# Kernel optimization log

Hardware: AMD Instinct MI355X
Metric: run time of the kernel (lower is better)

The kernel has to match this reference:

```python
import jax, jax.numpy as jnp
import numpy as np

N = 400_000      # total nodes
E = 6_400_000    # intra edges (avg degree 16)
B = 128          # graphs in batch
D = 35           # node_dim (pinned by the code)
DH = 2 * D       # 70 = attention dim
T = 140          # padded sequence length
SEQ = 2          # cat(lig,pro) [B,70] -> view(B,-1,35) => seq_len 2

# mask construction from forward() with sequence.size(1) == 2 (constant)
_m = np.eye(T, dtype=bool)
_m[SEQ:, :] = False
_m[:, SEQ:] = False
_m[:, SEQ - 1] = True
_m[SEQ - 1, :] = True
_m[SEQ - 1, SEQ - 1] = False
MASK = jnp.asarray(_m)  # [T,T] bool, broadcast over batch


def setup_inputs() -> dict:
    k = jax.random.split(jax.random.key(0), 24)
    s = 0.1
    return {
        "x": jax.random.normal(k[0], (N, D), jnp.float32),
        "edge_index": jax.random.randint(k[1], (2, E), 0, N),
        "split": jax.random.randint(k[2], (N,), 0, 2),
        "batch": jnp.sort(jax.random.randint(k[3], (N,), 0, B)),
        # 5 protein + 5 ligand GCNConv layers (weight [in,out], bias)
        "Wp": jax.random.normal(k[4], (5, D, D), jnp.float32) * s,
        "bp": jnp.zeros((5, D), jnp.float32),
        "Wl": jax.random.normal(k[5], (5, D, D), jnp.float32) * s,
        "bl": jnp.zeros((5, D), jnp.float32),
        # BiLSTM (torch layout: [4H, in]/[4H, H], gate order i,f,g,o)
        "wif": jax.random.normal(k[6], (4 * D, D), jnp.float32) * s,
        "whf": jax.random.normal(k[7], (4 * D, D), jnp.float32) * s,
        "bif": jnp.zeros((4 * D,), jnp.float32),
        "bhf": jnp.zeros((4 * D,), jnp.float32),
        "wib": jax.random.normal(k[8], (4 * D, D), jnp.float32) * s,
        "whb": jax.random.normal(k[9], (4 * D, D), jnp.float32) * s,
        "bib": jnp.zeros((4 * D,), jnp.float32),
        "bhb": jnp.zeros((4 * D,), jnp.float32),
        # single-head self-attention (70 -> 70) q/k/v/out projections
        "Wq": jax.random.normal(k[10], (DH, DH), jnp.float32) * s,
        "bq": jnp.zeros((DH,), jnp.float32),
        "Wk": jax.random.normal(k[11], (DH, DH), jnp.float32) * s,
        "bk": jnp.zeros((DH,), jnp.float32),
        "Wv": jax.random.normal(k[12], (DH, DH), jnp.float32) * s,
        "bv": jnp.zeros((DH,), jnp.float32),
        "Wo": jax.random.normal(k[13], (DH, DH), jnp.float32) * s,
        "bo": jnp.zeros((DH,), jnp.float32),
        # fc_in: Linear(9800,4340) + BatchNorm1d(4340) + Mish; fc_out: Linear(4340,1)
        "W1": jax.random.normal(k[14], (4340, 9800), jnp.float32) * 0.01,
        "b1": jnp.zeros((4340,), jnp.float32),
        "gamma": jnp.ones((4340,), jnp.float32),
        "beta": jnp.zeros((4340,), jnp.float32),
        "W2": jax.random.normal(k[15], (1, 4340), jnp.float32) * s,
        "b2": jnp.zeros((1,), jnp.float32),
    }


def _gcn_stack(x, src, dst, ew, Ws, bs):
    """5 stacked GCNConv + ReLU over a masked edge set (ew in {0,1} per edge).
    Matches PyG GCNConv: sym-normalized A+I, deg counted on active edges."""
    deg = jax.ops.segment_sum(ew, dst, num_segments=N) + 1.0  # +1 self loop
    dinv = jax.lax.rsqrt(deg)
    ecoef = (ew * dinv[src] * dinv[dst])[:, None]  # [E,1]
    scoef = (dinv * dinv)[:, None]                 # self-loop norm [N,1]
    h = x
    for i in range(5):
        t = h @ Ws[i]  # [N,D]
        agg = jax.ops.segment_sum(t[src] * ecoef, dst, num_segments=N)
        h = jax.nn.relu(agg + t * scoef + bs[i])
    return h


def _lstm(seq, wih, whh, b, reverse):
    # seq: [T, Bt, D] -> hidden states [T, Bt, D]
    def step(carry, xt):
        h, c = carry
        g = xt @ wih.T + h @ whh.T + b
        i, f, gg, o = jnp.split(g, 4, axis=-1)
        c = jax.nn.sigmoid(f) * c + jax.nn.sigmoid(i) * jnp.tanh(gg)
        h = jax.nn.sigmoid(o) * jnp.tanh(c)
        return (h, c), h
    h0 = jnp.zeros((seq.shape[1], D), seq.dtype)
    _, hs = jax.lax.scan(step, (h0, h0), seq, reverse=reverse)
    return hs


def _mish(x):
    return x * jnp.tanh(jax.nn.softplus(x))


def reference(x, edge_index, split, batch, Wp, bp, Wl, bl,
              wif, whf, bif, bhf, wib, whb, bib, bhb,
              Wq, bq, Wk, bk, Wv, bv, Wo, bo,
              W1, b1, gamma, beta, W2, b2):
    src, dst = edge_index[0], edge_index[1]
    wpro = (split[src] == 1).astype(x.dtype)  # edges whose source is protein
    wlig = 1.0 - wpro                          # edges whose source is ligand

    feat_pro = _gcn_stack(x, src, dst, wpro, Wp, bp)
    feat_lig = _gcn_stack(x, src, dst, wlig, Wl, bl)

    pro = jax.ops.segment_sum(feat_pro, batch, num_segments=B)  # [B,35]
    lig = jax.ops.segment_sum(feat_lig, batch, num_segments=B)

    seq = jnp.concatenate([lig, pro], axis=1).reshape(B, SEQ, D)  # [B,2,35]
    seq = jnp.pad(seq, ((0, 0), (0, T - SEQ), (0, 0)))            # [B,140,35]
    seq = seq.transpose(1, 0, 2)                                   # [T,B,35]

    hf = _lstm(seq, wif, whf, bif + bhf, False)
    hb = _lstm(seq, wib, whb, bib + bhb, True)
    out = jnp.concatenate([hf, hb], axis=-1).transpose(1, 0, 2)   # [B,140,70]

    q = out @ Wq.T + bq
    k = out @ Wk.T + bk
    v = out @ Wv.T + bv
    scores = jnp.einsum('btd,bsd->bts', q, k) / jnp.sqrt(jnp.float32(DH))
    scores = jnp.where(MASK, scores, jnp.float32(-1e9))
    ctx = jax.nn.softmax(scores, axis=-1) @ v                     # [B,140,70]
    ctx = ctx @ Wo.T + bo

    y = ctx.reshape(B, -1) @ W1.T + b1                            # [B,4340]
    mu = y.mean(0)
    var = ((y - mu) ** 2).mean(0)
    y = (y - mu) * jax.lax.rsqrt(var + 1e-5) * gamma + beta       # BN train mode
    y = _mish(y)
    return (y @ W2.T + b2).reshape(-1)                             # [B]
```

## Files before the change

kernel.cpp:

```cpp
#include <hip/hip_runtime.h>
#include <hip/hip_fp16.h>
#include <math.h>

#define DD 35
#define TT 140
#define DHX 70
#define GW 36
#define SLOT 48

__device__ __forceinline__ float sigf(float x){ return 1.0f/(1.0f+expf(-x)); }

__global__ void k_init(unsigned int* packed, int* bstart, int* bend,
                       float* out, const float* b2, int N, int B){
  int i = blockIdx.x*blockDim.x + threadIdx.x;
  if (i < N){ packed[i]=0u; }
  if (i < B){ bstart[i] = 0x7fffffff; bend[i] = 0; out[i] = b2[0]; }
}

__global__ void k_bitf(const int* __restrict__ split, unsigned int* bitf, int NW, int N){
  int w = blockIdx.x*blockDim.x + threadIdx.x;
  if (w >= NW) return;
  unsigned int m = 0;
  int base = w*32;
  int lim = N - base; if (lim > 32) lim = 32;
  for (int j=0;j<lim;++j) m |= (split[base+j]==1 ? 1u : 0u) << j;
  bitf[w] = m;
}

__global__ void k_fill2(const int* __restrict__ ei, const unsigned int* __restrict__ bitf,
                        unsigned int* packed, int* eidx, int E){
  int e = blockIdx.x*blockDim.x + threadIdx.x;
  if (e >= E) return;
  int s = __builtin_nontemporal_load(ei+e);
  int d = __builtin_nontemporal_load(ei+E+e);
  unsigned int bit = (bitf[s>>5] >> (s&31)) & 1u;
  unsigned int old = atomicAdd(&packed[d], bit ? 0x10000u : 1u);
  int slot = (int)((old>>16) + (old&0xFFFFu));
  if (slot < SLOT) eidx[(size_t)d*SLOT + slot] = (s<<1) | (int)bit;
}

__global__ void k_node1(const unsigned int* __restrict__ packed,
                        float* dinvp, float* dinvl,
                        const int* __restrict__ batch,
                        int* bstart, int* bend, int N){
  int i = blockIdx.x*blockDim.x + threadIdx.x;
  if (i >= N) return;
  unsigned int p = packed[i];
  int pc = (int)(p >> 16), lc = (int)(p & 0xFFFFu);
  dinvp[i] = rsqrtf((float)(pc + 1));
  dinvl[i] = rsqrtf((float)(lc + 1));
  int b = batch[i];
  if (i == 0 || batch[i-1] != b) bstart[b] = i;
  if (i == N-1 || batch[i+1] != b) bend[b] = i + 1;
}

__global__ void __launch_bounds__(256)
k_pack0(const float* __restrict__ x, const float* __restrict__ dinvp,
        const float* __restrict__ dinvl, const int* __restrict__ split,
        __half* __restrict__ gg, __half* __restrict__ own, int N){
  int node = blockIdx.x*4 + (threadIdx.x>>6);
  if (node >= N) return;
  int ln = threadIdx.x & 63;
  float v = (ln < DD)? x[(size_t)node*DD + ln] : 0.f;
  float dp = dinvp[node], dl = dinvl[node];
  int sel = split[node];
  float gv = (sel? dp : dl)*v;
  float ov = (sel? dl : dp)*v;
  float g0 = __shfl(gv,(2*ln)&63,64), g1 = __shfl(gv,(2*ln+1)&63,64);
  float o0 = __shfl(ov,(2*ln)&63,64), o1 = __shfl(ov,(2*ln+1)&63,64);
  if (ln < 18){
    *(__half2*)(gg  + (size_t)node*GW + 2*ln) = __floats2half2_rn(g0,g1);
    *(__half2*)(own + (size_t)node*GW + 2*ln) = __floats2half2_rn(o0,o1);
  }
}

__global__ void __launch_bounds__(256)
k_gcn(const __half* __restrict__ gg, const __half* __restrict__ own,
      __half* __restrict__ ggo, __half* __restrict__ owno,
      __half* __restrict__ hpF, __half* __restrict__ hlF,
      const unsigned int* __restrict__ packed, const int* __restrict__ eidx,
      const int* __restrict__ split,
      const float* __restrict__ dinvp, const float* __restrict__ dinvl,
      const float* __restrict__ Wp, const float* __restrict__ bp,
      const float* __restrict__ Wl, const float* __restrict__ bl,
      int N, int last){
  int node = blockIdx.x*4 + (threadIdx.x>>6);
  if (node >= N) return;
  int ln = threadIdx.x & 63;
  int sub = ln & 15, eo = ln >> 4;
  unsigned int pk = packed[node];
  int total = (int)((pk>>16) + (pk&0xFFFFu));
  if (total > SLOT) total = SLOT;
  int e0 = node*SLOT, e1 = e0 + total;
  float2 ap = {0.f,0.f}, al = {0.f,0.f};
  float2 tp = {0.f,0.f}, tl = {0.f,0.f};
  for (int e = e0; e < e1; e += 4){
    int idx = e + eo;
    bool val = idx < e1;
    int enc = val ? eidx[idx] : 0;
    const char* row = (const char*)gg + (size_t)(enc>>1)*(GW*2);
    unsigned int u = 0, ut = 0;
    if (val) u = *(const unsigned int*)(row + 4*sub);
    if (val && sub < 2) ut = *(const unsigned int*)(row + 64 + 4*sub);
    float ms = (val && (enc & 1)) ? 1.f : 0.f;
    float mo = (val && !(enc & 1)) ? 1.f : 0.f;
    float2 f  = __half22float2(*(__half2*)&u);
    float2 ft = __half22float2(*(__half2*)&ut);
    ap.x += ms*f.x;  ap.y += ms*f.y;  al.x += mo*f.x;  al.y += mo*f.y;
    tp.x += ms*ft.x; tp.y += ms*ft.y; tl.x += mo*ft.x; tl.y += mo*ft.y;
  }
  for (int off=16; off<64; off<<=1){
    ap.x += __shfl_xor(ap.x,off,64); ap.y += __shfl_xor(ap.y,off,64);
    al.x += __shfl_xor(al.x,off,64); al.y += __shfl_xor(al.y,off,64);
    tp.x += __shfl_xor(tp.x,off,64); tp.y += __shfl_xor(tp.y,off,64);
    tl.x += __shfl_xor(tl.x,off,64); tl.y += __shfl_xor(tl.y,off,64);
  }
  int srcl = ln>>1, odd = ln&1;
  float px = __shfl(ap.x, srcl, 64), py = __shfl(ap.y, srcl, 64);
  float lx = __shfl(al.x, srcl, 64), ly = __shfl(al.y, srcl, 64);
  float zp = odd? py : px;
  float zl = odd? ly : lx;
  float tpx0 = __shfl(tp.x,0,64), tpy0 = __shfl(tp.y,0,64), tpx1 = __shfl(tp.x,1,64);
  float tlx0 = __shfl(tl.x,0,64), tly0 = __shfl(tl.y,0,64), tlx1 = __shfl(tl.x,1,64);
  if (ln == 32){ zp = tpx0; zl = tlx0; }
  else if (ln == 33){ zp = tpy0; zl = tly0; }
  else if (ln == 34){ zp = tpx1; zl = tlx1; }
  int sel = split[node];
  float dp = dinvp[node], dl = dinvl[node];
  float sg = 0.f, so = 0.f;
  if (ln < DD){
    sg = __half2float(gg [(size_t)node*GW + ln]);
    so = __half2float(own[(size_t)node*GW + ln]);
  }
  float selfp = sel ? sg : so;
  float selfl = sel ? so : sg;
  bool act = ln < DD;
  float zpf = act ? dp*(zp + selfp) : 0.f;
  float zlf = act ? dl*(zl + selfl) : 0.f;
  float op = 0.f, ol = 0.f;
  for (int j=0;j<DD;++j){
    float zpj = __shfl(zpf, j, 64);
    float zlj = __shfl(zlf, j, 64);
    float wp = act ? Wp[j*DD+ln] : 0.f;
    float wl = act ? Wl[j*DD+ln] : 0.f;
    op += zpj*wp; ol += zlj*wl;
  }
  float opb = act ? fmaxf(op + bp[ln], 0.f) : 0.f;
  float olb = act ? fmaxf(ol + bl[ln], 0.f) : 0.f;
  if (last){
    float a0 = __shfl(opb,(2*ln)&63,64), a1 = __shfl(opb,(2*ln+1)&63,64);
    float b0 = __shfl(olb,(2*ln)&63,64), b1 = __shfl(olb,(2*ln+1)&63,64);
    if (ln < 18){
      *(__half2*)(hpF + (size_t)node*GW + 2*ln) = __floats2half2_rn(a0,a1);
      *(__half2*)(hlF + (size_t)node*GW + 2*ln) = __floats2half2_rn(b0,b1);
    }
  } else {
    float ggv  = sel ? dp*opb : dl*olb;
    float ownv = sel ? dl*olb : dp*opb;
    float a0 = __shfl(ggv,(2*ln)&63,64), a1 = __shfl(ggv,(2*ln+1)&63,64);
    float b0 = __shfl(ownv,(2*ln)&63,64), b1 = __shfl(ownv,(2*ln+1)&63,64);
    if (ln < 18){
      *(__half2*)(ggo  + (size_t)node*GW + 2*ln) = __floats2half2_rn(a0,a1);
      *(__half2*)(owno + (size_t)node*GW + 2*ln) = __floats2half2_rn(b0,b1);
    }
  }
}

__global__ void k_bsum(const __half* __restrict__ gp, const __half* __restrict__ gl,
                       const int* __restrict__ bstart, const int* __restrict__ bend,
                       float* pro, float* lig){
  __shared__ float sp[4][GW], sl[4][GW];
  int b = blockIdx.x;
  int w = threadIdx.x>>6, ln = threadIdx.x&63;
  int s0 = bstart[b], s1 = bend[b];
  float apx=0.f, apy=0.f, alx=0.f, aly=0.f;
  if (ln < 18){
    for (int n=s0+w; n<s1; n+=4){
      float2 a = __half22float2(*(const __half2*)(gp + (size_t)n*GW + 2*ln));
      float2 c = __half22float2(*(const __half2*)(gl + (size_t)n*GW + 2*ln));
      apx+=a.x; apy+=a.y; alx+=c.x; aly+=c.y;
    }
    sp[w][2*ln]=apx; sp[w][2*ln+1]=apy;
    sl[w][2*ln]=alx; sl[w][2*ln+1]=aly;
  }
  __syncthreads();
  if (threadIdx.x < DD){
    int d = threadIdx.x;
    pro[b*DD+d] = sp[0][d]+sp[1][d]+sp[2][d]+sp[3][d];
    lig[b*DD+d] = sl[0][d]+sl[1][d]+sl[2][d]+sl[3][d];
  }
}

__global__ void k_lstm_common(const float* __restrict__ wib, const float* __restrict__ whb,
                              const float* __restrict__ bib, const float* __restrict__ bhb,
                              float* hbc, float* hbcst){
  __shared__ float h[DD], cc[DD], g[4*DD];
  int t = threadIdx.x;
  if (t < DD){ h[t]=0.f; cc[t]=0.f; }
  __syncthreads();
  for (int k=1;k<=TT-2;++k){
    if (t < 4*DD){
      float acc = bib[t]+bhb[t];
      for (int m=0;m<DD;++m) acc += whb[t*DD+m]*h[m];
      g[t]=acc;
    }
    __syncthreads();
    if (t < DD){
      float ig=g[t], fg=g[DD+t], gg=g[2*DD+t], og=g[3*DD+t];
      float cv = sigf(fg)*cc[t] + sigf(ig)*tanhf(gg);
      float hv = sigf(og)*tanhf(cv);
      cc[t]=cv; h[t]=hv;
      hbc[(TT-k)*DD + t] = hv;
    }
    __syncthreads();
  }
  if (t<DD){ hbcst[t]=h[t]; hbcst[DD+t]=cc[t]; }
}

__global__ void k_lstm_batch(const float* __restrict__ lig, const float* __restrict__ pro,
   const float* __restrict__ wif, const float* __restrict__ whf,
   const float* __restrict__ bif, const float* __restrict__ bhf,
   const float* __restrict__ wib, const float* __restrict__ whb,
   const float* __restrict__ bib, const float* __restrict__ bhb,
   const float* __restrict__ hbc, const float* __restrict__ hbcst, float* outseq){
  __shared__ float x0[DD], x1[DD], h[DD], cc[DD], g[4*DD], xg0[4*DD], xg1[4*DD];
  int b = blockIdx.x, t = threadIdx.x;
  if (t<DD){ x0[t]=lig[b*DD+t]; x1[t]=pro[b*DD+t]; h[t]=0.f; cc[t]=0.f; }
  __syncthreads();
  if (t<4*DD){
    float a0=0.f, a1=0.f;
    for (int m=0;m<DD;++m){ a0 += wif[t*DD+m]*x0[m]; a1 += wif[t*DD+m]*x1[m]; }
    xg0[t]=a0; xg1[t]=a1;
  }
  __syncthreads();
  float* outb = outseq + (size_t)b*TT*DHX;
  for (int tt=0;tt<TT;++tt){
    if (t<4*DD){
      float acc = bif[t]+bhf[t] + (tt==0? xg0[t] : (tt==1? xg1[t] : 0.f));
      for (int m=0;m<DD;++m) acc += whf[t*DD+m]*h[m];
      g[t]=acc;
    }
    __syncthreads();
    if (t<DD){
      float ig=g[t], fg=g[DD+t], gg=g[2*DD+t], og=g[3*DD+t];
      float cv = sigf(fg)*cc[t]+sigf(ig)*tanhf(gg);
      float hv = sigf(og)*tanhf(cv);
      cc[t]=cv; h[t]=hv;
      outb[tt*DHX + t] = hv;
    }
    __syncthreads();
  }
  if (t<4*DD){
    float a0=0.f, a1=0.f;
    for (int m=0;m<DD;++m){ a0 += wib[t*DD+m]*x0[m]; a1 += wib[t*DD+m]*x1[m]; }
    xg0[t]=a0; xg1[t]=a1;
  }
  if (t<DD){ h[t]=hbcst[t]; cc[t]=hbcst[DD+t]; }
  __syncthreads();
  for (int step=0; step<2; ++step){
    int tt = 1-step;
    if (t<4*DD){
      float acc = bib[t]+bhb[t] + (tt==1? xg1[t] : xg0[t]);
      for (int m=0;m<DD;++m) acc += whb[t*DD+m]*h[m];
      g[t]=acc;
    }
    __syncthreads();
    if (t<DD){
      float ig=g[t], fg=g[DD+t], gg=g[2*DD+t], og=g[3*DD+t];
      float cv = sigf(fg)*cc[t]+sigf(ig)*tanhf(gg);
      float hv = sigf(og)*tanhf(cv);
      cc[t]=cv; h[t]=hv;
      outb[tt*DHX + DD + t] = hv;
    }
    __syncthreads();
  }
  for (int idx=t; idx<(TT-2)*DD; idx+=blockDim.x){
    int tt = 2 + idx/DD, d = idx%DD;
    outb[tt*DHX + DD + d] = hbc[tt*DD + d];
  }
}

__global__ void __launch_bounds__(256)
k_attn(const float* __restrict__ outseq,
  const float* __restrict__ Wq, const float* __restrict__ bq,
  const float* __restrict__ Wk, const float* __restrict__ bk,
  const float* __restrict__ Wv, const float* __restrict__ bv,
  const float* __restrict__ Wo, const float* __restrict__ bo,
  float* PT, int B){
  __shared__ float so[TT*DHX];
  __shared__ float sk[TT*DHX];
  __shared__ float sv[TT*DHX];
  __shared__ float sq[2*DHX];
  __shared__ float es[TT];
  __shared__ float red[4];
  __shared__ float ctx[3*DHX];
  int b = blockIdx.x, tid = threadIdx.x;
  const float* ob = outseq + (size_t)b*TT*DHX;
  for (int i=tid;i<TT*DHX;i+=256) so[i]=ob[i];
  __syncthreads();
  for (int i=tid;i<TT*DHX;i+=256){
    int s=i/DHX, d=i%DHX;
    float ak=bk[d], av=bv[d];
    const float* r = so + s*DHX;
    for (int j=0;j<DHX;++j){ float o=r[j]; ak += o*Wk[d*DHX+j]; av += o*Wv[d*DHX+j]; }
    sk[i]=ak; sv[i]=av;
  }
  for (int i=tid;i<2*DHX;i+=256){
    int s=i/DHX, d=i%DHX;
    float a=bq[d];
    for (int j=0;j<DHX;++j) a += so[s*DHX+j]*Wq[d*DHX+j];
    sq[i]=a;
  }
  __syncthreads();
  const float scale = 0.11952286093343936f;
  for (int s=tid;s<TT;s+=256){
    float a=0.f;
    for (int j=0;j<DHX;++j) a += sq[DHX+j]*sk[s*DHX+j];
    es[s] = a*scale;
  }
  __syncthreads();
  if (tid < 64){
    float m=-1e30f;
    for (int s=tid;s<TT;s+=64) if (s!=1) m=fmaxf(m, es[s]);
    for (int o=32;o;o>>=1) m = fmaxf(m, __shfl_xor(m,o,64));
    if (tid==0) red[0]=m;
  }
  __syncthreads();
  float m = red[0];
  for (int s=tid;s<TT;s+=256) es[s] = (s==1)? 0.f : expf(es[s]-m);
  __syncthreads();
  if (tid<64){
    float sum=0.f;
    for (int s=tid;s<TT;s+=64) sum+=es[s];
    for (int o=32;o;o>>=1) sum += __shfl_xor(sum,o,64);
    if (tid==0) red[1]=sum;
  }
  if (tid==0){
    float s00=0.f,s01=0.f;
    for (int j=0;j<DHX;++j){ s00 += sq[j]*sk[j]; s01 += sq[j]*sk[DHX+j]; }
    s00*=scale; s01*=scale;
    float mm=fmaxf(s00,s01);
    float e0=expf(s00-mm), e1=expf(s01-mm);
    red[2]=e0/(e0+e1); red[3]=e1/(e0+e1);
  }
  __syncthreads();
  float inv = 1.0f/red[1];
  float a0=red[2], a1=red[3];
  if (tid < DHX){
    int d=tid;
    float c1=0.f;
    for (int s=0;s<TT;++s) c1 += es[s]*sv[s*DHX+d];
    ctx[DHX+d] = c1*inv;
    ctx[d] = a0*sv[d] + a1*sv[DHX+d];
    ctx[2*DHX+d] = sv[DHX+d];
  }
  __syncthreads();
  for (int i=tid;i<3*DHX;i+=256){
    int tt=i/DHX, d=i%DHX;
    float a=bo[d];
    const float* cv = ctx + tt*DHX;
    for (int j=0;j<DHX;++j) a += Wo[d*DHX+j]*cv[j];
    PT[(size_t)i*B + b] = a;
  }
}

__global__ void k_w1s(const float* __restrict__ W1, float* w1s){
  __shared__ float sh[DHX];
  int j = blockIdx.x; int tid = threadIdx.x;
  int d = tid % DHX, half = tid / DHX;
  const float* r = W1 + (size_t)j*(TT*DHX);
  float acc = 0.f;
  int t0 = half ? 71 : 2, t1 = half ? 140 : 71;
  for (int t=t0; t<t1; ++t) acc += r[t*DHX+d];
  if (half==0) sh[d] = acc;
  __syncthreads();
  if (half) w1s[(size_t)j*DHX+d] = sh[d] + acc;
}

__global__ void k_y(const float* __restrict__ PT, const float* __restrict__ W1,
                    const float* __restrict__ w1s, const float* __restrict__ b1,
                    float* yT, int B){
  int j = blockIdx.x; int b = threadIdx.x;
  const float* r = W1 + (size_t)j*(TT*DHX);
  float acc = b1[j];
  for (int i=0;i<2*DHX;++i) acc += r[i]*PT[(size_t)i*B+b];
  const float* rs = w1s + (size_t)j*DHX;
  for (int i=0;i<DHX;++i) acc += rs[i]*PT[(size_t)(2*DHX+i)*B+b];
  yT[(size_t)j*B+b] = acc;
}

__global__ void k_bn(const float* __restrict__ yT, const float* __restrict__ gamma,
                     const float* __restrict__ beta, const float* __restrict__ W2,
                     float* out, int B, int J){
  __shared__ float red_s[2];
  int b = threadIdx.x;
  int lane = b & 63, w = b>>6;
  float acc = 0.f;
  int j0 = blockIdx.x*32;
  float invB = 1.0f/(float)B;
  for (int jj=0;jj<32;++jj){
    int j = j0+jj; if (j>=J) break;
    float v = yT[(size_t)j*B + b];
    float s=v;
    for (int o=32;o;o>>=1) s += __shfl_xor(s,o,64);
    if (lane==0) red_s[w]=s;
    __syncthreads();
    float mu = (red_s[0]+red_s[1]) * invB;
    __syncthreads();
    float dd = v-mu;
    float q=dd*dd;
    for (int o=32;o;o>>=1) q += __shfl_xor(q,o,64);
    if (lane==0) red_s[w]=q;
    __syncthreads();
    float var = (red_s[0]+red_s[1]) * invB;
    __syncthreads();
    float xn = dd*rsqrtf(var+1e-5f)*gamma[j]+beta[j];
    float sp = (xn>20.f)? xn : log1pf(expf(xn));
    float mish = xn*tanhf(sp);
    acc += mish*W2[j];
  }
  atomicAdd(&out[b], acc);
}

extern "C" void kernel_launch(void* const* d_in, const int* in_sizes, int n_in,
                              void* d_out, int out_size, void* d_ws, size_t ws_size,
                              hipStream_t stream)
{
  const float* x    = (const float*)d_in[0];
  const int*   ei   = (const int*)  d_in[1];
  const int*   split= (const int*)  d_in[2];
  const int*   batch= (const int*)  d_in[3];
  const float* Wp   = (const float*)d_in[4];
  const float* bp   = (const float*)d_in[5];
  const float* Wl   = (const float*)d_in[6];
  const float* bl   = (const float*)d_in[7];
  const float* wif  = (const float*)d_in[8];
  const float* whf  = (const float*)d_in[9];
  const float* bif  = (const float*)d_in[10];
  const float* bhf  = (const float*)d_in[11];
  const float* wib  = (const float*)d_in[12];
  const float* whb  = (const float*)d_in[13];
  const float* bib  = (const float*)d_in[14];
  const float* bhb  = (const float*)d_in[15];
  const float* Wq   = (const float*)d_in[16];
  const float* bq   = (const float*)d_in[17];
  const float* Wk   = (const float*)d_in[18];
  const float* bk   = (const float*)d_in[19];
  const float* Wv   = (const float*)d_in[20];
  const float* bv   = (const float*)d_in[21];
  const float* Wo   = (const float*)d_in[22];
  const float* bo   = (const float*)d_in[23];
  const float* W1   = (const float*)d_in[24];
  const float* b1   = (const float*)d_in[25];
  const float* gam  = (const float*)d_in[26];
  const float* bet  = (const float*)d_in[27];
  const float* W2   = (const float*)d_in[28];
  const float* b2   = (const float*)d_in[29];
  float* out = (float*)d_out;

  const int N = in_sizes[0]/DD;
  const int E = in_sizes[1]/2;
  const int B = out_size;
  const int J = in_sizes[25];
  (void)n_in; (void)ws_size;

  char* ws = (char*)d_ws;
  size_t off_ = 0;
  auto carve = [&](size_t bytes)->void*{ void* p = ws + off_; off_ = (off_ + bytes + 255) & ~(size_t)255; return p; };
  __half* ggA  = (__half*)carve((size_t)N*GW*2);
  __half* ownA = (__half*)carve((size_t)N*GW*2);
  __half* ggB  = (__half*)carve((size_t)N*GW*2);
  __half* ownB = (__half*)carve((size_t)N*GW*2);
  int*   eidx  = (int*)  carve((size_t)N*SLOT*4);
  float* dinvp = (float*)carve((size_t)N*4);
  float* dinvl = (float*)carve((size_t)N*4);
  unsigned int* packed = (unsigned int*)carve((size_t)N*4);
  unsigned int* bitf   = (unsigned int*)carve((size_t)((N+31)/32)*4);
  float* pro   = (float*)carve((size_t)B*DD*4);
  float* lig   = (float*)carve((size_t)B*DD*4);
  int*   bstart= (int*)  carve((size_t)B*4);
  int*   bend  = (int*)  carve((size_t)B*4);
  float* hbc   = (float*)carve((size_t)TT*DD*4);
  float* hbcst = (float*)carve(2*DD*4);
  float* outseq= (float*)carve((size_t)B*TT*DHX*4);
  float* PT    = (float*)carve((size_t)3*DHX*B*4);
  float* w1s   = (float*)carve((size_t)J*DHX*4);
  float* yT    = (float*)carve((size_t)J*B*4);

  int mx = (N>B)?N:B;
  int NW = (N+31)/32;
  k_init<<<(mx+255)/256, 256, 0, stream>>>(packed, bstart, bend, out, b2, N, B);
  k_bitf<<<(NW+255)/256, 256, 0, stream>>>(split, bitf, NW, N);
  k_fill2<<<(E+255)/256, 256, 0, stream>>>(ei, bitf, packed, eidx, E);
  k_node1<<<(N+255)/256, 256, 0, stream>>>(packed, dinvp, dinvl, batch, bstart, bend, N);
  k_pack0<<<(N+3)/4, 256, 0, stream>>>(x, dinvp, dinvl, split, ggA, ownA, N);

  const __half* ggi = ggA; const __half* owni = ownA;
  __half* ggo = ggB; __half* owno = ownB;
  __half* hpF = nullptr; __half* hlF = nullptr;
  for (int L=0; L<5; ++L){
    int last = (L==4);
    if (last){ hpF = ggo; hlF = owno; }
    k_gcn<<<(N+3)/4, 256, 0, stream>>>(ggi, owni, ggo, owno, ggo, owno,
      packed, eidx, split, dinvp, dinvl,
      Wp + (size_t)L*DD*DD, bp + (size_t)L*DD, Wl + (size_t)L*DD*DD, bl + (size_t)L*DD,
      N, last);
    const __half* t1 = ggi; ggi = ggo; ggo = (__half*)t1;
    const __half* t2 = owni; owni = owno; owno = (__half*)t2;
  }

  k_bsum<<<B, 256, 0, stream>>>(hpF, hlF, bstart, bend, pro, lig);
  k_lstm_common<<<1, 192, 0, stream>>>(wib, whb, bib, bhb, hbc, hbcst);
  k_lstm_batch<<<B, 192, 0, stream>>>(lig, pro, wif, whf, bif, bhf, wib, whb, bib, bhb, hbc, hbcst, outseq);
  k_attn<<<B, 256, 0, stream>>>(outseq, Wq, bq, Wk, bk, Wv, bv, Wo, bo, PT, B);
  k_w1s<<<J, 140, 0, stream>>>(W1, w1s);
  k_y<<<J, B, 0, stream>>>(PT, W1, w1s, b1, yT, B);
  k_bn<<<(J+31)/32, B, 0, stream>>>(yT, gam, bet, W2, out, B, J);
}
```

Baseline: 3.817 ms.

## Pack gathered GCN features into 64-byte block-floating-point rows

Replaces the fp16 gathered-feature rows (72 bytes) with a custom per-row shared-exponent format: 14-bit integer mantissas packed two per 32-bit word, plus a 4-bit exponent and nibble-packed tail columns, for 64 bytes per row. The edge-gather loop does one aligned 4-byte load per lane and decodes with integer shifts, aiming to cut gather bandwidth and load count. The final-layer outputs go to separate buffers. The cost is extra encode and decode arithmetic, and reduced precision, especially for the three tail features.

```diff
diff --git a/kernel.cpp b/kernel.cpp
--- a/kernel.cpp
+++ b/kernel.cpp
@@ -9,6 +9,26 @@
 #define SLOT 48
 
 __device__ __forceinline__ float sigf(float x){ return 1.0f/(1.0f+expf(-x)); }
+
+__device__ __forceinline__ void encode_row(float v, int ln, unsigned int* dst){
+  float av = fabsf(v);
+  for (int o=32;o;o>>=1) av = fmaxf(av, __shfl_xor(av,o,64));
+  int e = ((__float_as_int(av)>>23)&255) - 127;
+  int Ep = e < -8 ? -8 : (e > 7 ? 7 : e);
+  float invs = __int_as_float((139 - Ep)<<23);
+  int m = (int)rintf(v*invs);
+  m = m < -8191 ? -8191 : (m > 8191 ? 8191 : m);
+  int mt = (int)rintf(v*invs*0.25f) + 2048;
+  mt = mt < 0 ? 0 : (mt > 4095 ? 4095 : mt);
+  int mB  = __shfl(m, (ln+16)&63, 64);
+  int t32 = __shfl(mt, 32, 64), t33 = __shfl(mt, 33, 64), t34 = __shfl(mt, 34, 64);
+  if (ln < 16){
+    int tt = (ln<3)? t32 : (ln<6)? t33 : t34;
+    int p  = (ln<3)? ln : (ln<6)? ln-3 : ln-6;
+    int nib = (ln<9) ? ((tt>>(4*p))&15) : (ln==15 ? (Ep+8) : 0);
+    dst[ln] = ((unsigned)m & 0x3FFFu) | (((unsigned)mB & 0x3FFFu)<<14) | ((unsigned)nib<<28);
+  }
+}
 
 __global__ void k_init(unsigned int* packed, int* bstart, int* bend,
                        float* out, const float* b2, int N, int B){
@@ -57,7 +77,7 @@
 __global__ void __launch_bounds__(256)
 k_pack0(const float* __restrict__ x, const float* __restrict__ dinvp,
         const float* __restrict__ dinvl, const int* __restrict__ split,
-        __half* __restrict__ gg, __half* __restrict__ own, int N){
+        unsigned int* __restrict__ gg, __half* __restrict__ own, int N){
   int node = blockIdx.x*4 + (threadIdx.x>>6);
   if (node >= N) return;
   int ln = threadIdx.x & 63;
@@ -66,17 +86,14 @@
   int sel = split[node];
   float gv = (sel? dp : dl)*v;
   float ov = (sel? dl : dp)*v;
-  float g0 = __shfl(gv,(2*ln)&63,64), g1 = __shfl(gv,(2*ln+1)&63,64);
+  encode_row((ln<DD)? gv : 0.f, ln, gg + (size_t)node*16);
   float o0 = __shfl(ov,(2*ln)&63,64), o1 = __shfl(ov,(2*ln+1)&63,64);
-  if (ln < 18){
-    *(__half2*)(gg  + (size_t)node*GW + 2*ln) = __floats2half2_rn(g0,g1);
-    *(__half2*)(own + (size_t)node*GW + 2*ln) = __floats2half2_rn(o0,o1);
-  }
+  if (ln < 18) *(__half2*)(own + (size_t)node*GW + 2*ln) = __floats2half2_rn(o0,o1);
 }
 
 __global__ void __launch_bounds__(256)
-k_gcn(const __half* __restrict__ gg, const __half* __restrict__ own,
-      __half* __restrict__ ggo, __half* __restrict__ owno,
+k_gcn(const unsigned int* __restrict__ gg, const __half* __restrict__ own,
+      unsigned int* __restrict__ ggo, __half* __restrict__ owno,
       __half* __restrict__ hpF, __half* __restrict__ hlF,
       const unsigned int* __restrict__ packed, const int* __restrict__ eidx,
       const int* __restrict__ split,
@@ -87,51 +104,63 @@
   int node = blockIdx.x*4 + (threadIdx.x>>6);
   if (node >= N) return;
   int ln = threadIdx.x & 63;
-  int sub = ln & 15, eo = ln >> 4;
+  int sub = ln & 15;
+  int grp = ln >> 4;
   unsigned int pk = packed[node];
   int total = (int)((pk>>16) + (pk&0xFFFFu));
   if (total > SLOT) total = SLOT;
   int e0 = node*SLOT, e1 = e0 + total;
-  float2 ap = {0.f,0.f}, al = {0.f,0.f};
-  float2 tp = {0.f,0.f}, tl = {0.f,0.f};
+
+  float aP0=0.f, aP1=0.f, aL0=0.f, aL1=0.f;
+  float aPt=0.f, aLt=0.f;
   for (int e = e0; e < e1; e += 4){
-    int idx = e + eo;
+    int idx = e + grp;
     bool val = idx < e1;
     int enc = val ? eidx[idx] : 0;
-    const char* row = (const char*)gg + (size_t)(enc>>1)*(GW*2);
-    unsigned int u = 0, ut = 0;
-    if (val) u = *(const unsigned int*)(row + 4*sub);
-    if (val && sub < 2) ut = *(const unsigned int*)(row + 64 + 4*sub);
-    float ms = (val && (enc & 1)) ? 1.f : 0.f;
-    float mo = (val && !(enc & 1)) ? 1.f : 0.f;
-    float2 f  = __half22float2(*(__half2*)&u);
-    float2 ft = __half22float2(*(__half2*)&ut);
-    ap.x += ms*f.x;  ap.y += ms*f.y;  al.x += mo*f.x;  al.y += mo*f.y;
-    tp.x += ms*ft.x; tp.y += ms*ft.y; tl.x += mo*ft.x; tl.y += mo*ft.y;
+    unsigned int u = val ? gg[(size_t)(enc>>1)*16 + sub] : 0u;
+    int uE = __shfl((int)u, (ln & 48) | 15, 64);
+    float s = val ? __int_as_float(((((unsigned)uE)>>28) + 107) << 23) : 0.f;
+    float sp = (enc & 1) ? s : 0.f;
+    float sl = (enc & 1) ? 0.f : s;
+    int m0 = ((int)(u<<18))>>18;
+    int m1 = ((int)(u<<4))>>18;
+    float f0 = (float)m0, f1 = (float)m1;
+    aP0 += sp*f0; aP1 += sp*f1; aL0 += sl*f0; aL1 += sl*f1;
+    float nv = (sub == 9) ? 1.0f : (float)(u>>28);
+    aPt += sp*nv; aLt += sl*nv;
   }
   for (int off=16; off<64; off<<=1){
-    ap.x += __shfl_xor(ap.x,off,64); ap.y += __shfl_xor(ap.y,off,64);
-    al.x += __shfl_xor(al.x,off,64); al.y += __shfl_xor(al.y,off,64);
-    tp.x += __shfl_xor(tp.x,off,64); tp.y += __shfl_xor(tp.y,off,64);
-    tl.x += __shfl_xor(tl.x,off,64); tl.y += __shfl_xor(tl.y,off,64);
-  }
-  int srcl = ln>>1, odd = ln&1;
-  float px = __shfl(ap.x, srcl, 64), py = __shfl(ap.y, srcl, 64);
-  float lx = __shfl(al.x, srcl, 64), ly = __shfl(al.y, srcl, 64);
-  float zp = odd? py : px;
-  float zl = odd? ly : lx;
-  float tpx0 = __shfl(tp.x,0,64), tpy0 = __shfl(tp.y,0,64), tpx1 = __shfl(tp.x,1,64);
-  float tlx0 = __shfl(tl.x,0,64), tly0 = __shfl(tl.y,0,64), tlx1 = __shfl(tl.x,1,64);
-  if (ln == 32){ zp = tpx0; zl = tlx0; }
-  else if (ln == 33){ zp = tpy0; zl = tly0; }
-  else if (ln == 34){ zp = tpx1; zl = tlx1; }
+    aP0 += __shfl_xor(aP0,off,64); aP1 += __shfl_xor(aP1,off,64);
+    aL0 += __shfl_xor(aL0,off,64); aL1 += __shfl_xor(aL1,off,64);
+    aPt += __shfl_xor(aPt,off,64); aLt += __shfl_xor(aLt,off,64);
+  }
+  float a0 = __shfl(aP0, ln&15, 64), a1 = __shfl(aP1, ln&15, 64);
+  float b0 = __shfl(aL0, ln&15, 64), b1 = __shfl(aL1, ln&15, 64);
+  int tb = (ln>=32 && ln<35) ? (ln-32)*3 : 0;
+  float q0p=__shfl(aPt,tb,64), q1p=__shfl(aPt,tb+1,64), q2p=__shfl(aPt,tb+2,64);
+  float q0l=__shfl(aLt,tb,64), q1l=__shfl(aLt,tb+1,64), q2l=__shfl(aLt,tb+2,64);
+  float Sp = __shfl(aPt, 9, 64), Sl = __shfl(aLt, 9, 64);
+  float vtp = 4.f*(q0p + 16.f*q1p + 256.f*q2p - 2048.f*Sp);
+  float vtl = 4.f*(q0l + 16.f*q1l + 256.f*q2l - 2048.f*Sl);
+  float zp = (ln<16)? a0 : (ln<32)? a1 : vtp;
+  float zl = (ln<16)? b0 : (ln<32)? b1 : vtl;
   int sel = split[node];
   float dp = dinvp[node], dl = dinvl[node];
+  const unsigned int* rowS = gg + (size_t)node*16;
+  unsigned int wE = rowS[15];
+  float ss = __int_as_float((int)(((wE>>28) + 107) << 23));
   float sg = 0.f, so = 0.f;
-  if (ln < DD){
-    sg = __half2float(gg [(size_t)node*GW + ln]);
-    so = __half2float(own[(size_t)node*GW + ln]);
-  }
+  if (ln < 32){
+    unsigned int w = rowS[sub];
+    int m = (ln<16)? (((int)(w<<18))>>18) : (((int)(w<<4))>>18);
+    sg = (float)m * ss;
+  } else if (ln < DD){
+    int t = ln-32;
+    unsigned int w0=rowS[3*t], w1=rowS[3*t+1], w2=rowS[3*t+2];
+    int mp = (int)(w0>>28) | ((int)(w1>>28)<<4) | ((int)(w2>>28)<<8);
+    sg = (float)(mp - 2048) * ss * 4.f;
+  }
+  if (ln < DD) so = __half2float(own[(size_t)node*GW + ln]);
   float selfp = sel ? sg : so;
   float selfl = sel ? so : sg;
   bool act = ln < DD;
@@ -148,21 +177,19 @@
   float opb = act ? fmaxf(op + bp[ln], 0.f) : 0.f;
   float olb = act ? fmaxf(ol + bl[ln], 0.f) : 0.f;
   if (last){
-    float a0 = __shfl(opb,(2*ln)&63,64), a1 = __shfl(opb,(2*ln+1)&63,64);
-    float b0 = __shfl(olb,(2*ln)&63,64), b1 = __shfl(olb,(2*ln+1)&63,64);
+    float c0 = __shfl(opb,(2*ln)&63,64), c1 = __shfl(opb,(2*ln+1)&63,64);
+    float d0 = __shfl(olb,(2*ln)&63,64), d1 = __shfl(olb,(2*ln+1)&63,64);
     if (ln < 18){
-      *(__half2*)(hpF + (size_t)node*GW + 2*ln) = __floats2half2_rn(a0,a1);
-      *(__half2*)(hlF + (size_t)node*GW + 2*ln) = __floats2half2_rn(b0,b1);
+      *(__half2*)(hpF + (size_t)node*GW + 2*ln) = __floats2half2_rn(c0,c1);
+      *(__half2*)(hlF + (size_t)node*GW + 2*ln) = __floats2half2_rn(d0,d1);
     }
   } else {
     float ggv  = sel ? dp*opb : dl*olb;
     float ownv = sel ? dl*olb : dp*opb;
-    float a0 = __shfl(ggv,(2*ln)&63,64), a1 = __shfl(ggv,(2*ln+1)&63,64);
-    float b0 = __shfl(ownv,(2*ln)&63,64), b1 = __shfl(ownv,(2*ln+1)&63,64);
-    if (ln < 18){
-      *(__half2*)(ggo  + (size_t)node*GW + 2*ln) = __floats2half2_rn(a0,a1);
-      *(__half2*)(owno + (size_t)node*GW + 2*ln) = __floats2half2_rn(b0,b1);
-    }
+    encode_row(act? ggv : 0.f, ln, ggo + (size_t)node*16);
+    float d0 = __shfl(ownv,(2*ln)&63,64), d1 = __shfl(ownv,(2*ln+1)&63,64);
+    if (ln < 18)
+      *(__half2*)(owno + (size_t)node*GW + 2*ln) = __floats2half2_rn(d0,d1);
   }
 }
 
@@ -467,10 +494,12 @@
   char* ws = (char*)d_ws;
   size_t off_ = 0;
   auto carve = [&](size_t bytes)->void*{ void* p = ws + off_; off_ = (off_ + bytes + 255) & ~(size_t)255; return p; };
-  __half* ggA  = (__half*)carve((size_t)N*GW*2);
+  unsigned int* ggA = (unsigned int*)carve((size_t)N*16*4);
+  unsigned int* ggB = (unsigned int*)carve((size_t)N*16*4);
   __half* ownA = (__half*)carve((size_t)N*GW*2);
-  __half* ggB  = (__half*)carve((size_t)N*GW*2);
   __half* ownB = (__half*)carve((size_t)N*GW*2);
+  __half* hpF  = (__half*)carve((size_t)N*GW*2);
+  __half* hlF  = (__half*)carve((size_t)N*GW*2);
   int*   eidx  = (int*)  carve((size_t)N*SLOT*4);
   float* dinvp = (float*)carve((size_t)N*4);
   float* dinvl = (float*)carve((size_t)N*4);
@@ -495,17 +524,15 @@
   k_node1<<<(N+255)/256, 256, 0, stream>>>(packed, dinvp, dinvl, batch, bstart, bend, N);
   k_pack0<<<(N+3)/4, 256, 0, stream>>>(x, dinvp, dinvl, split, ggA, ownA, N);
 
-  const __half* ggi = ggA; const __half* owni = ownA;
-  __half* ggo = ggB; __half* owno = ownB;
-  __half* hpF = nullptr; __half* hlF = nullptr;
+  const unsigned int* ggi = ggA; const __half* owni = ownA;
+  unsigned int* ggo = ggB; __half* owno = ownB;
   for (int L=0; L<5; ++L){
     int last = (L==4);
-    if (last){ hpF = ggo; hlF = owno; }
-    k_gcn<<<(N+3)/4, 256, 0, stream>>>(ggi, owni, ggo, owno, ggo, owno,
+    k_gcn<<<(N+3)/4, 256, 0, stream>>>(ggi, owni, ggo, owno, hpF, hlF,
       packed, eidx, split, dinvp, dinvl,
       Wp + (size_t)L*DD*DD, bp + (size_t)L*DD, Wl + (size_t)L*DD*DD, bl + (size_t)L*DD,
       N, last);
-    const __half* t1 = ggi; ggi = ggo; ggo = (__half*)t1;
+    const unsigned int* t1 = ggi; ggi = ggo; ggo = (unsigned int*)t1;
     const __half* t2 = owni; owni = owno; owno = (__half*)t2;
   }
 
```

After: 3.949 ms. 3.4% more time.

## Split gathered GCN features into 64B-aligned row plus tail array; merge small kernels

Applied to the files above, without the earlier changes.

The gathered half-precision feature rows go from a 72-byte stride to a 64-byte main array plus a separate 8-byte tail array. Each gathered neighbour row then fits one aligned 64-byte segment instead of straddling cache lines, with the three tail features fetched as a single 8-byte load by one lane. The bitfield build is folded into the init kernel, and the W1 column-sum kernel is merged with the LSTM-common kernel so that work runs alongside the long serial LSTM block. This adds dedicated final-layer output buffers and a second scattered load per edge for the tail.

```diff
diff --git a/kernel.cpp b/kernel.cpp
--- a/kernel.cpp
+++ b/kernel.cpp
@@ -11,20 +11,19 @@
 __device__ __forceinline__ float sigf(float x){ return 1.0f/(1.0f+expf(-x)); }
 
 __global__ void k_init(unsigned int* packed, int* bstart, int* bend,
-                       float* out, const float* b2, int N, int B){
+                       float* out, const float* b2,
+                       const int* __restrict__ split, unsigned int* bitf,
+                       int N, int B, int NW){
   int i = blockIdx.x*blockDim.x + threadIdx.x;
   if (i < N){ packed[i]=0u; }
   if (i < B){ bstart[i] = 0x7fffffff; bend[i] = 0; out[i] = b2[0]; }
-}
-
-__global__ void k_bitf(const int* __restrict__ split, unsigned int* bitf, int NW, int N){
-  int w = blockIdx.x*blockDim.x + threadIdx.x;
-  if (w >= NW) return;
-  unsigned int m = 0;
-  int base = w*32;
-  int lim = N - base; if (lim > 32) lim = 32;
-  for (int j=0;j<lim;++j) m |= (split[base+j]==1 ? 1u : 0u) << j;
-  bitf[w] = m;
+  if (i < NW){
+    unsigned int m = 0;
+    int base = i*32;
+    int lim = N - base; if (lim > 32) lim = 32;
+    for (int j=0;j<lim;++j) m |= (split[base+j]==1 ? 1u : 0u) << j;
+    bitf[i] = m;
+  }
 }
 
 __global__ void k_fill2(const int* __restrict__ ei, const unsigned int* __restrict__ bitf,
@@ -57,7 +56,7 @@
 __global__ void __launch_bounds__(256)
 k_pack0(const float* __restrict__ x, const float* __restrict__ dinvp,
         const float* __restrict__ dinvl, const int* __restrict__ split,
-        __half* __restrict__ gg, __half* __restrict__ own, int N){
+        __half* __restrict__ gg, __half* __restrict__ tt, __half* __restrict__ own, int N){
   int node = blockIdx.x*4 + (threadIdx.x>>6);
   if (node >= N) return;
   int ln = threadIdx.x & 63;
@@ -68,15 +67,23 @@
   float ov = (sel? dl : dp)*v;
   float g0 = __shfl(gv,(2*ln)&63,64), g1 = __shfl(gv,(2*ln+1)&63,64);
   float o0 = __shfl(ov,(2*ln)&63,64), o1 = __shfl(ov,(2*ln+1)&63,64);
-  if (ln < 18){
-    *(__half2*)(gg  + (size_t)node*GW + 2*ln) = __floats2half2_rn(g0,g1);
+  float t32 = __shfl(gv,32,64), t33 = __shfl(gv,33,64), t34 = __shfl(gv,34,64);
+  if (ln < 16)
+    *(__half2*)(gg + (size_t)node*32 + 2*ln) = __floats2half2_rn(g0,g1);
+  if (ln == 16){
+    __half2 a = __floats2half2_rn(t32,t33);
+    __half2 b = __floats2half2_rn(t34,0.f);
+    uint2 u; u.x = *(unsigned int*)&a; u.y = *(unsigned int*)&b;
+    *(uint2*)(tt + (size_t)node*4) = u;
+  }
+  if (ln < 18)
     *(__half2*)(own + (size_t)node*GW + 2*ln) = __floats2half2_rn(o0,o1);
-  }
 }
 
 __global__ void __launch_bounds__(256)
-k_gcn(const __half* __restrict__ gg, const __half* __restrict__ own,
-      __half* __restrict__ ggo, __half* __restrict__ owno,
+k_gcn(const __half* __restrict__ gg, const __half* __restrict__ tt,
+      const __half* __restrict__ own,
+      __half* __restrict__ ggo, __half* __restrict__ tto, __half* __restrict__ owno,
       __half* __restrict__ hpF, __half* __restrict__ hlF,
       const unsigned int* __restrict__ packed, const int* __restrict__ eidx,
       const int* __restrict__ split,
@@ -94,44 +101,48 @@
   int e0 = node*SLOT, e1 = e0 + total;
   float2 ap = {0.f,0.f}, al = {0.f,0.f};
   float2 tp = {0.f,0.f}, tl = {0.f,0.f};
+  float tq = 0.f, tr = 0.f;
   for (int e = e0; e < e1; e += 4){
     int idx = e + eo;
     bool val = idx < e1;
     int enc = val ? eidx[idx] : 0;
-    const char* row = (const char*)gg + (size_t)(enc>>1)*(GW*2);
-    unsigned int u = 0, ut = 0;
-    if (val) u = *(const unsigned int*)(row + 4*sub);
-    if (val && sub < 2) ut = *(const unsigned int*)(row + 64 + 4*sub);
+    unsigned int rb = ((unsigned int)(enc>>1))<<6;
+    unsigned int u = 0;
+    uint2 ut = {0u,0u};
+    if (val) u = *(const unsigned int*)((const char*)gg + rb + (sub<<2));
+    if (val && sub == 0) ut = *(const uint2*)((const char*)tt + (((unsigned int)(enc>>1))<<3));
     float ms = (val && (enc & 1)) ? 1.f : 0.f;
     float mo = (val && !(enc & 1)) ? 1.f : 0.f;
-    float2 f  = __half22float2(*(__half2*)&u);
-    float2 ft = __half22float2(*(__half2*)&ut);
-    ap.x += ms*f.x;  ap.y += ms*f.y;  al.x += mo*f.x;  al.y += mo*f.y;
-    tp.x += ms*ft.x; tp.y += ms*ft.y; tl.x += mo*ft.x; tl.y += mo*ft.y;
+    float2 f   = __half22float2(*(__half2*)&u);
+    float2 f01 = __half22float2(*(__half2*)&ut.x);
+    float2 f2  = __half22float2(*(__half2*)&ut.y);
+    ap.x += ms*f.x;   ap.y += ms*f.y;   al.x += mo*f.x;   al.y += mo*f.y;
+    tp.x += ms*f01.x; tp.y += ms*f01.y; tq += ms*f2.x;
+    tl.x += mo*f01.x; tl.y += mo*f01.y; tr += mo*f2.x;
   }
   for (int off=16; off<64; off<<=1){
     ap.x += __shfl_xor(ap.x,off,64); ap.y += __shfl_xor(ap.y,off,64);
     al.x += __shfl_xor(al.x,off,64); al.y += __shfl_xor(al.y,off,64);
     tp.x += __shfl_xor(tp.x,off,64); tp.y += __shfl_xor(tp.y,off,64);
     tl.x += __shfl_xor(tl.x,off,64); tl.y += __shfl_xor(tl.y,off,64);
+    tq += __shfl_xor(tq,off,64); tr += __shfl_xor(tr,off,64);
   }
   int srcl = ln>>1, odd = ln&1;
   float px = __shfl(ap.x, srcl, 64), py = __shfl(ap.y, srcl, 64);
   float lx = __shfl(al.x, srcl, 64), ly = __shfl(al.y, srcl, 64);
   float zp = odd? py : px;
   float zl = odd? ly : lx;
-  float tpx0 = __shfl(tp.x,0,64), tpy0 = __shfl(tp.y,0,64), tpx1 = __shfl(tp.x,1,64);
-  float tlx0 = __shfl(tl.x,0,64), tly0 = __shfl(tl.y,0,64), tlx1 = __shfl(tl.x,1,64);
-  if (ln == 32){ zp = tpx0; zl = tlx0; }
-  else if (ln == 33){ zp = tpy0; zl = tly0; }
-  else if (ln == 34){ zp = tpx1; zl = tlx1; }
+  float tpx = __shfl(tp.x,0,64), tpy = __shfl(tp.y,0,64), tqz = __shfl(tq,0,64);
+  float tlx = __shfl(tl.x,0,64), tly = __shfl(tl.y,0,64), trz = __shfl(tr,0,64);
+  if (ln == 32){ zp = tpx; zl = tlx; }
+  else if (ln == 33){ zp = tpy; zl = tly; }
+  else if (ln == 34){ zp = tqz; zl = trz; }
   int sel = split[node];
   float dp = dinvp[node], dl = dinvl[node];
   float sg = 0.f, so = 0.f;
-  if (ln < DD){
-    sg = __half2float(gg [(size_t)node*GW + ln]);
-    so = __half2float(own[(size_t)node*GW + ln]);
-  }
+  if (ln < 32) sg = __half2float(gg[(size_t)node*32 + ln]);
+  else if (ln < DD) sg = __half2float(tt[(size_t)node*4 + (ln-32)]);
+  if (ln < DD) so = __half2float(own[(size_t)node*GW + ln]);
   float selfp = sel ? sg : so;
   float selfl = sel ? so : sg;
   bool act = ln < DD;
@@ -159,10 +170,17 @@
     float ownv = sel ? dl*olb : dp*opb;
     float a0 = __shfl(ggv,(2*ln)&63,64), a1 = __shfl(ggv,(2*ln+1)&63,64);
     float b0 = __shfl(ownv,(2*ln)&63,64), b1 = __shfl(ownv,(2*ln+1)&63,64);
-    if (ln < 18){
-      *(__half2*)(ggo  + (size_t)node*GW + 2*ln) = __floats2half2_rn(a0,a1);
+    float t2 = __shfl(ggv,32,64), t3 = __shfl(ggv,33,64), t4 = __shfl(ggv,34,64);
+    if (ln < 16)
+      *(__half2*)(ggo + (size_t)node*32 + 2*ln) = __floats2half2_rn(a0,a1);
+    if (ln == 16){
+      __half2 ha = __floats2half2_rn(t2,t3);
+      __half2 hb = __floats2half2_rn(t4,0.f);
+      uint2 u2; u2.x = *(unsigned int*)&ha; u2.y = *(unsigned int*)&hb;
+      *(uint2*)(tto + (size_t)node*4) = u2;
+    }
+    if (ln < 18)
       *(__half2*)(owno + (size_t)node*GW + 2*ln) = __floats2half2_rn(b0,b1);
-    }
   }
 }
 
@@ -191,11 +209,28 @@
   }
 }
 
-__global__ void k_lstm_common(const float* __restrict__ wib, const float* __restrict__ whb,
-                              const float* __restrict__ bib, const float* __restrict__ bhb,
-                              float* hbc, float* hbcst){
+__global__ void k_misc(const float* __restrict__ W1, float* w1s,
+                       const float* __restrict__ wib, const float* __restrict__ whb,
+                       const float* __restrict__ bib, const float* __restrict__ bhb,
+                       float* hbc, float* hbcst, int J){
+  __shared__ float sh[DHX];
   __shared__ float h[DD], cc[DD], g[4*DD];
-  int t = threadIdx.x;
+  int tid = threadIdx.x;
+  if ((int)blockIdx.x < J){
+    int j = blockIdx.x;
+    int d = tid % DHX, half = tid / DHX;
+    float acc = 0.f;
+    if (tid < 140){
+      const float* r = W1 + (size_t)j*(TT*DHX);
+      int t0 = half ? 71 : 2, t1 = half ? 140 : 71;
+      for (int t=t0; t<t1; ++t) acc += r[t*DHX+d];
+      if (half==0) sh[d] = acc;
+    }
+    __syncthreads();
+    if (tid < 140 && half==1) w1s[(size_t)j*DHX+d] = sh[d] + acc;
+    return;
+  }
+  int t = tid;
   if (t < DD){ h[t]=0.f; cc[t]=0.f; }
   __syncthreads();
   for (int k=1;k<=TT-2;++k){
@@ -206,8 +241,8 @@
     }
     __syncthreads();
     if (t < DD){
-      float ig=g[t], fg=g[DD+t], gg=g[2*DD+t], og=g[3*DD+t];
-      float cv = sigf(fg)*cc[t] + sigf(ig)*tanhf(gg);
+      float ig=g[t], fg=g[DD+t], gg2=g[2*DD+t], og=g[3*DD+t];
+      float cv = sigf(fg)*cc[t] + sigf(ig)*tanhf(gg2);
       float hv = sigf(og)*tanhf(cv);
       cc[t]=cv; h[t]=hv;
       hbc[(TT-k)*DD + t] = hv;
@@ -362,19 +397,6 @@
     for (int j=0;j<DHX;++j) a += Wo[d*DHX+j]*cv[j];
     PT[(size_t)i*B + b] = a;
   }
-}
-
-__global__ void k_w1s(const float* __restrict__ W1, float* w1s){
-  __shared__ float sh[DHX];
-  int j = blockIdx.x; int tid = threadIdx.x;
-  int d = tid % DHX, half = tid / DHX;
-  const float* r = W1 + (size_t)j*(TT*DHX);
-  float acc = 0.f;
-  int t0 = half ? 71 : 2, t1 = half ? 140 : 71;
-  for (int t=t0; t<t1; ++t) acc += r[t*DHX+d];
-  if (half==0) sh[d] = acc;
-  __syncthreads();
-  if (half) w1s[(size_t)j*DHX+d] = sh[d] + acc;
 }
 
 __global__ void k_y(const float* __restrict__ PT, const float* __restrict__ W1,
@@ -467,10 +489,14 @@
   char* ws = (char*)d_ws;
   size_t off_ = 0;
   auto carve = [&](size_t bytes)->void*{ void* p = ws + off_; off_ = (off_ + bytes + 255) & ~(size_t)255; return p; };
-  __half* ggA  = (__half*)carve((size_t)N*GW*2);
+  __half* ggA  = (__half*)carve((size_t)N*32*2);
+  __half* ggB  = (__half*)carve((size_t)N*32*2);
+  __half* ttA  = (__half*)carve((size_t)N*4*2);
+  __half* ttB  = (__half*)carve((size_t)N*4*2);
   __half* ownA = (__half*)carve((size_t)N*GW*2);
-  __half* ggB  = (__half*)carve((size_t)N*GW*2);
   __half* ownB = (__half*)carve((size_t)N*GW*2);
+  __half* hpF  = (__half*)carve((size_t)N*GW*2);
+  __half* hlF  = (__half*)carve((size_t)N*GW*2);
   int*   eidx  = (int*)  carve((size_t)N*SLOT*4);
   float* dinvp = (float*)carve((size_t)N*4);
   float* dinvl = (float*)carve((size_t)N*4);
@@ -489,31 +515,28 @@
 
   int mx = (N>B)?N:B;
   int NW = (N+31)/32;
-  k_init<<<(mx+255)/256, 256, 0, stream>>>(packed, bstart, bend, out, b2, N, B);
-  k_bitf<<<(NW+255)/256, 256, 0, stream>>>(split, bitf, NW, N);
+  k_init<<<(mx+255)/256, 256, 0, stream>>>(packed, bstart, bend, out, b2, split, bitf, N, B, NW);
   k_fill2<<<(E+255)/256, 256, 0, stream>>>(ei, bitf, packed, eidx, E);
   k_node1<<<(N+255)/256, 256, 0, stream>>>(packed, dinvp, dinvl, batch, bstart, bend, N);
-  k_pack0<<<(N+3)/4, 256, 0, stream>>>(x, dinvp, dinvl, split, ggA, ownA, N);
-
-  const __half* ggi = ggA; const __half* owni = ownA;
-  __half* ggo = ggB; __half* owno = ownB;
-  __half* hpF = nullptr; __half* hlF = nullptr;
+  k_pack0<<<(N+3)/4, 256, 0, stream>>>(x, dinvp, dinvl, split, ggA, ttA, ownA, N);
+
+  const __half* ggi = ggA; const __half* tti = ttA; const __half* owni = ownA;
+  __half* ggo = ggB; __half* tto = ttB; __half* owno = ownB;
   for (int L=0; L<5; ++L){
     int last = (L==4);
-    if (last){ hpF = ggo; hlF = owno; }
-    k_gcn<<<(N+3)/4, 256, 0, stream>>>(ggi, owni, ggo, owno, ggo, owno,
+    k_gcn<<<(N+3)/4, 256, 0, stream>>>(ggi, tti, owni, ggo, tto, owno, hpF, hlF,
       packed, eidx, split, dinvp, dinvl,
       Wp + (size_t)L*DD*DD, bp + (size_t)L*DD, Wl + (size_t)L*DD*DD, bl + (size_t)L*DD,
       N, last);
     const __half* t1 = ggi; ggi = ggo; ggo = (__half*)t1;
-    const __half* t2 = owni; owni = owno; owno = (__half*)t2;
+    const __half* t2 = tti; tti = tto; tto = (__half*)t2;
+    const __half* t3 = owni; owni = owno; owno = (__half*)t3;
   }
 
   k_bsum<<<B, 256, 0, stream>>>(hpF, hlF, bstart, bend, pro, lig);
-  k_lstm_common<<<1, 192, 0, stream>>>(wib, whb, bib, bhb, hbc, hbcst);
+  k_misc<<<J+1, 192, 0, stream>>>(W1, w1s, wib, whb, bib, bhb, hbc, hbcst, J);
   k_lstm_batch<<<B, 192, 0, stream>>>(lig, pro, wif, whf, bif, bhf, wib, whb, bib, bhb, hbc, hbcst, outseq);
   k_attn<<<B, 256, 0, stream>>>(outseq, Wq, bq, Wk, bk, Wv, bv, Wo, bo, PT, B);
-  k_w1s<<<J, 140, 0, stream>>>(W1, w1s);
   k_y<<<J, B, 0, stream>>>(PT, W1, w1s, b1, yT, B);
   k_bn<<<(J+31)/32, B, 0, stream>>>(yT, gam, bet, W2, out, B, J);
 }
```

New measurement: 3.998 ms. 1.05x slower.
